# Optimization experiments

Measured on AMD Instinct MI355X. Metric: run time of the kernel, lower is better.

## Reference

```python
import jax, jax.numpy as jnp
import numpy as np

D_MODEL = 1024
HEADS = 16
HEAD_DIM = D_MODEL // HEADS
EPS = 1e-6


def feature_map(x):
    # F.elu(x) + 1
    return jax.nn.elu(x) + 1.0


def setup_inputs() -> dict:
    key = jax.random.key(0)
    ks = jax.random.split(key, 9)
    B, N, D = 4, 4096, D_MODEL
    s = 1.0 / np.sqrt(D)
    return {
        "x": jax.random.normal(ks[0], (B, N, D), dtype=jnp.float32),
        "Wq": jax.random.normal(ks[1], (D, D), dtype=jnp.float32) * s,
        "bq": jnp.zeros((D,), dtype=jnp.float32),
        "Wk": jax.random.normal(ks[2], (D, D), dtype=jnp.float32) * s,
        "bk": jnp.zeros((D,), dtype=jnp.float32),
        "Wv": jax.random.normal(ks[3], (D, D), dtype=jnp.float32) * s,
        "bv": jnp.zeros((D,), dtype=jnp.float32),
        "Wo": jax.random.normal(ks[4], (D, D), dtype=jnp.float32) * s,
        "bo": jnp.zeros((D,), dtype=jnp.float32),
    }


def reference(x, Wq, bq, Wk, bk, Wv, bv, Wo, bo):
    B, N, D = x.shape
    H, hd = HEADS, HEAD_DIM
    # torch Linear: y = x @ W.T + b
    q = feature_map((x @ Wq.T + bq).reshape(B, N, H, hd))
    k = feature_map((x @ Wk.T + bk).reshape(B, N, H, hd))
    v = (x @ Wv.T + bv).reshape(B, N, H, hd)
    k_sum = k.sum(axis=1)                                   # (B, H, hd)
    D_inv = 1.0 / (jnp.einsum('bnhd,bhd->bnh', q, k_sum) + EPS)
    context = jnp.einsum('bnhd,bnhv->bhdv', k, v)            # (B, H, hd, hd)
    out = jnp.einsum('bnhd,bhdv->bnhv', q, context) * D_inv[..., None]
    out = out.reshape(B, N, D)
    return out @ Wo.T + bo
```

## Files before the change

### kernel.cpp

```cpp
#include <hip/hip_runtime.h>
#include <hip/hip_bf16.h>

typedef __attribute__((ext_vector_type(8))) short bf16x8;
typedef __attribute__((ext_vector_type(4))) float f32x4;

__device__ __forceinline__ float b2f(unsigned short u) {
  union { unsigned int i; float f; } x; x.i = ((unsigned int)u) << 16; return x.f;
}
__device__ __forceinline__ unsigned short f2b(float f) {
  union { __hip_bfloat16 h; unsigned short u; } x; x.h = __float2bfloat16(f); return x.u;
}
__device__ __forceinline__ f32x4 mfma16(bf16x8 a, bf16x8 b, f32x4 c) {
  return __builtin_amdgcn_mfma_f32_16x16x32_bf16(a, b, c, 0, 0, 0);
}
__device__ __forceinline__ void gl16(const void* g, void* l) {
  __builtin_amdgcn_global_load_lds(
      (const __attribute__((address_space(1))) unsigned int*)g,
      (__attribute__((address_space(3))) unsigned int*)l, 16, 0, 0);
}

__global__ __launch_bounds__(256) void cast_k(const float* __restrict__ src,
                                              unsigned short* __restrict__ dst, int n4) {
  int i = blockIdx.x * 256 + threadIdx.x;
  if (i >= n4) return;
  float4 v = ((const float4*)src)[i];
  ushort4 o;
  o.x = f2b(v.x); o.y = f2b(v.y); o.z = f2b(v.z); o.w = f2b(v.w);
  ((ushort4*)dst)[i] = o;
}

__global__ __launch_bounds__(256) void castw_k(
    const float* __restrict__ s0, const float* __restrict__ s1,
    const float* __restrict__ s2, const float* __restrict__ s3,
    unsigned short* __restrict__ d0, unsigned short* __restrict__ d1,
    unsigned short* __restrict__ d2, unsigned short* __restrict__ d3) {
  int seg = blockIdx.x >> 10;
  int i = (blockIdx.x & 1023) * 256 + threadIdx.x;
  const float* s = (seg == 0) ? s0 : (seg == 1) ? s1 : (seg == 2) ? s2 : s3;
  unsigned short* d = (seg == 0) ? d0 : (seg == 1) ? d1 : (seg == 2) ? d2 : d3;
  float4 v = ((const float4*)s)[i];
  ushort4 o;
  o.x = f2b(v.x); o.y = f2b(v.y); o.z = f2b(v.z); o.w = f2b(v.w);
  ((ushort4*)d)[i] = o;
}

#define BARX() asm volatile("s_barrier" ::: "memory")
#define LGKM0() asm volatile("s_waitcnt lgkmcnt(0)" ::: "memory")
#define WAITV4() asm volatile("s_waitcnt vmcnt(4)" ::: "memory")
#define WAITV0() asm volatile("s_waitcnt vmcnt(0)" ::: "memory")
#define P1() __builtin_amdgcn_s_setprio(1)
#define P0() __builtin_amdgcn_s_setprio(0)

#define STAGE_A(BUF, G, TAU) do { \
  gl16(gA_0 + (size_t)(G) * 65536 + (TAU) * 64, sAB + (BUF) * 32768 + (G) * 16384 + u0 * 16); \
  gl16(gA_1 + (size_t)(G) * 65536 + (TAU) * 64, sAB + (BUF) * 32768 + (G) * 16384 + u1 * 16); } while (0)
#define STAGE_B(BUF, G, TAU) do { \
  gl16(gB_0 + (size_t)(G) * 32768 + (TAU) * 64, sAB + 65536 + (BUF) * 32768 + (G) * 16384 + u0 * 16); \
  gl16(gB_1 + (size_t)(G) * 32768 + (TAU) * 64, sAB + 65536 + (BUF) * 32768 + (G) * 16384 + u1 * 16); } while (0)

#define LOAD_A(BUF, MH) do { \
  _Pragma("unroll") for (int mi = 0; mi < 4; ++mi) { \
    const char* p_ = (const char*)sAB + (BUF) * 32768 + (MH) * 16384 + aRd + mi * 2048; \
    af[mi][0] = *(const bf16x8*)(p_ + sr0); \
    af[mi][1] = *(const bf16x8*)(p_ + sr1); } } while (0)
#define LOAD_B(BUF, NH, DST) do { \
  _Pragma("unroll") for (int ni = 0; ni < 2; ++ni) { \
    const char* p_ = (const char*)sAB + 65536 + (BUF) * 32768 + (NH) * 16384 + bRd + ni * 2048; \
    DST[ni][0] = *(const bf16x8*)(p_ + sr0); \
    DST[ni][1] = *(const bf16x8*)(p_ + sr1); } } while (0)

#define QUAD(MH, NH, BF) do { \
  _Pragma("unroll") for (int mi = 0; mi < 4; ++mi) \
    _Pragma("unroll") for (int ni = 0; ni < 2; ++ni) { \
      acc[(MH) * 4 + mi][(NH) * 2 + ni] = mfma16(af[mi][0], BF[ni][0], acc[(MH) * 4 + mi][(NH) * 2 + ni]); \
      acc[(MH) * 4 + mi][(NH) * 2 + ni] = mfma16(af[mi][1], BF[ni][1], acc[(MH) * 4 + mi][(NH) * 2 + ni]); } } while (0)

template<int MODE>
__global__ __launch_bounds__(512, 2) void gemm256(
    const unsigned short* __restrict__ A,
    const unsigned short* __restrict__ W0, const unsigned short* __restrict__ W1,
    const unsigned short* __restrict__ W2,
    const float* __restrict__ bias0, const float* __restrict__ bias1, const float* __restrict__ bias2,
    float* __restrict__ outF,
    unsigned short* __restrict__ o0, unsigned short* __restrict__ o1, unsigned short* __restrict__ o2,
    int tiles_n, float* __restrict__ ksum)
{
  __shared__ char sAB[131072];
  int bid = blockIdx.x;
  int nwg = gridDim.x;
  int cpx = nwg >> 3;
  int sbid = (bid & 7) * cpx + (bid >> 3);
  int tn = sbid % tiles_n, tm = sbid / tiles_n;
  int m0 = tm * 256, n0 = tn * 256;

  const unsigned short* W = W0; const float* bias = bias0; unsigned short* outB = o0;
  int sel = 0;
  if (MODE == 1) {
    sel = n0 >> 10;
    if (sel == 1) { W = W1; bias = bias1; outB = o1; }
    else if (sel == 2) { W = W2; bias = bias2; outB = o2; }
  } else {
    W = W0 + ((size_t)(m0 >> 12) << 20);
  }
  int nloc0 = (MODE == 1) ? (n0 & 1023) : n0;

  int t = threadIdx.x, w = t >> 6, l = t & 63;
  int wm = w >> 2, wn = w & 3;

  int u0 = t, u1 = t + 512;
  int lr0 = u0 >> 3, lr1 = u1 >> 3;
  int sl0 = (u0 & 7) ^ (lr0 & 7), sl1 = (u1 & 7) ^ (lr1 & 7);
  int rA0 = ((lr0 >> 6) << 7) + (lr0 & 63), rA1 = ((lr1 >> 6) << 7) + (lr1 & 63);
  int rB0 = ((lr0 >> 5) << 6) + (lr0 & 31), rB1 = ((lr1 >> 5) << 6) + (lr1 & 31);
  const unsigned short* gA_0 = A + (size_t)(m0 + rA0) * 1024 + sl0 * 8;
  const unsigned short* gA_1 = A + (size_t)(m0 + rA1) * 1024 + sl1 * 8;
  const unsigned short* gB_0 = W + (size_t)(nloc0 + rB0) * 1024 + sl0 * 8;
  const unsigned short* gB_1 = W + (size_t)(nloc0 + rB1) * 1024 + sl1 * 8;

  int aRd = (wm * 64 + (l & 15)) * 128;
  int bRd = (wn * 32 + (l & 15)) * 128;
  int sr0 = (((l >> 4) + 0) ^ (l & 7)) * 16;
  int sr1 = (((l >> 4) + 4) ^ (l & 7)) * 16;

  f32x4 acc[8][4];
  f32x4 zero = {0.f, 0.f, 0.f, 0.f};
#pragma unroll
  for (int i = 0; i < 8; ++i)
#pragma unroll
    for (int jx = 0; jx < 4; ++jx) acc[i][jx] = zero;
  bf16x8 af[4][2], bf0[2][2], bf1[2][2];

  STAGE_A(0, 0, 0); STAGE_B(0, 0, 0); STAGE_A(0, 1, 0); STAGE_B(0, 1, 0);
  STAGE_A(1, 0, 1); STAGE_B(1, 0, 1);
  WAITV4();
  BARX();

  for (int j = 0; j < 8; ++j) {
    int t1 = 2 * j + 1;
    int t2 = (j < 7) ? (2 * j + 2) : 14;
    int t3 = (j < 7) ? (2 * j + 3) : 15;
    LOAD_A(0, 0); LOAD_B(0, 0, bf0);
    STAGE_A(1, 1, t1);
    BARX(); LGKM0(); P1(); QUAD(0, 0, bf0); P0(); BARX();
    LOAD_B(0, 1, bf1);
    STAGE_B(1, 1, t1);
    BARX(); LGKM0(); P1(); QUAD(0, 1, bf1); P0(); BARX();
    LOAD_A(0, 1);
    STAGE_A(0, 0, t2);
    BARX(); LGKM0(); P1(); QUAD(1, 0, bf0); P0(); BARX();
    STAGE_B(0, 0, t2);
    BARX(); LGKM0(); P1(); QUAD(1, 1, bf1); P0(); WAITV4(); BARX();
    LOAD_A(1, 0); LOAD_B(1, 0, bf0);
    STAGE_A(0, 1, t2);
    BARX(); LGKM0(); P1(); QUAD(0, 0, bf0); P0(); BARX();
    LOAD_B(1, 1, bf1);
    STAGE_B(0, 1, t2);
    BARX(); LGKM0(); P1(); QUAD(0, 1, bf1); P0(); BARX();
    LOAD_A(1, 1);
    STAGE_A(1, 0, t3);
    BARX(); LGKM0(); P1(); QUAD(1, 0, bf0); P0(); BARX();
    STAGE_B(1, 0, t3);
    BARX(); LGKM0(); P1(); QUAD(1, 1, bf1); P0(); WAITV4(); BARX();
  }
  WAITV0();

  if (MODE == 1 && sel >= 1) {
    int b_idx = m0 >> 12;
    int nloc_h = nloc0 >> 6;
#pragma unroll
    for (int mq = 0; mq < 8; ++mq) {
      int r_base = wm * 128 + (mq >> 2) * 64 + (mq & 3) * 16 + ((l >> 4) << 2);
#pragma unroll
      for (int nq = 0; nq < 4; ++nq) {
        int c_loc = wn * 64 + (nq >> 1) * 32 + (nq & 1) * 16 + (l & 15);
        float bb = bias[nloc0 + c_loc];
        float v0 = acc[mq][nq][0] + bb, v1 = acc[mq][nq][1] + bb;
        float v2 = acc[mq][nq][2] + bb, v3 = acc[mq][nq][3] + bb;
        if (sel == 1) {
          v0 = (v0 > 0.0f) ? (v0 + 1.0f) : __expf(v0);
          v1 = (v1 > 0.0f) ? (v1 + 1.0f) : __expf(v1);
          v2 = (v2 > 0.0f) ? (v2 + 1.0f) : __expf(v2);
          v3 = (v3 > 0.0f) ? (v3 + 1.0f) : __expf(v3);
        }
        unsigned long long pk =
            (unsigned long long)(f2b(v0) | ((unsigned int)f2b(v1) << 16)) |
            ((unsigned long long)(f2b(v2) | ((unsigned int)f2b(v3) << 16)) << 32);
        int byte = c_loc * 512 + ((r_base * 2) ^ ((c_loc & 7) << 4));
        *(unsigned long long*)(sAB + byte) = pk;
      }
    }
    __syncthreads();
#pragma unroll
    for (int qq = 0; qq < 16; ++qq) {
      int c_loc = qq * 16 + w * 2 + (l >> 5);
      int n_off = (l & 31) * 8;
      int d = c_loc & 63;
      int bh = b_idx * 16 + nloc_h + (c_loc >> 6);
      int byte = c_loc * 512 + ((n_off * 2) ^ ((c_loc & 7) << 4));
      bf16x8 ch = *(const bf16x8*)(sAB + byte);
      *(bf16x8*)(outB + (size_t)(bh * 64 + d) * 4096 + (m0 & 4095) + n_off) = ch;
      if (sel == 1) {
        float s = 0.f;
#pragma unroll
        for (int jj = 0; jj < 8; ++jj) s += b2f((unsigned short)ch[jj]);
        s += __shfl_xor(s, 1);
        s += __shfl_xor(s, 2);
        s += __shfl_xor(s, 4);
        s += __shfl_xor(s, 8);
        s += __shfl_xor(s, 16);
        if ((l & 31) == 0) atomicAdd(ksum + bh * 64 + d, s);
      }
    }
  } else {
#pragma unroll
    for (int mq = 0; mq < 8; ++mq) {
      int grow = m0 + wm * 128 + (mq >> 2) * 64 + (mq & 3) * 16 + ((l >> 4) << 2);
#pragma unroll
      for (int nq = 0; nq < 4; ++nq) {
        int gcol = n0 + wn * 64 + (nq >> 1) * 32 + (nq & 1) * 16 + (l & 15);
        if (MODE == 0) {
          float bb = bias[gcol];
#pragma unroll
          for (int r = 0; r < 4; ++r)
            outF[(size_t)(grow + r) * 1024 + gcol] = acc[mq][nq][r] + bb;
        } else {
          int c = gcol & 1023;
          float bb = bias[c];
#pragma unroll
          for (int r = 0; r < 4; ++r) {
            float v = acc[mq][nq][r] + bb;
            v = (v > 0.0f) ? (v + 1.0f) : __expf(v);
            outB[(size_t)(grow + r) * 1024 + c] = f2b(v);
          }
        }
      }
    }
  }
}

__global__ __launch_bounds__(256) void ctx_gemm(
    const unsigned short* __restrict__ kT,
    const unsigned short* __restrict__ vT,
    float* __restrict__ ctxT)
{
  __shared__ float red[4][64 * 65];
  int bid = blockIdx.x;
  int bh = bid >> 3, ch = bid & 7;
  int t = threadIdx.x, wv = t >> 6, l = t & 63;
  int noff = ch * 512 + wv * 128 + ((l >> 4) << 3);
  const unsigned short* aB = kT + ((size_t)bh * 64 + (l & 15)) * 4096 + noff;
  const unsigned short* bB = vT + ((size_t)bh * 64 + (l & 15)) * 4096 + noff;
  f32x4 acc[4][4];
  f32x4 zero = {0.f, 0.f, 0.f, 0.f};
#pragma unroll
  for (int i = 0; i < 4; ++i)
#pragma unroll
    for (int j = 0; j < 4; ++j) acc[i][j] = zero;
  for (int ks = 0; ks < 4; ++ks) {
    bf16x8 av[4], bv[4];
#pragma unroll
    for (int mi = 0; mi < 4; ++mi) av[mi] = *(const bf16x8*)(aB + (size_t)mi * 16 * 4096 + ks * 32);
#pragma unroll
    for (int ni = 0; ni < 4; ++ni) bv[ni] = *(const bf16x8*)(bB + (size_t)ni * 16 * 4096 + ks * 32);
#pragma unroll
    for (int mi = 0; mi < 4; ++mi)
#pragma unroll
      for (int ni = 0; ni < 4; ++ni)
        acc[mi][ni] = mfma16(av[mi], bv[ni], acc[mi][ni]);
  }
#pragma unroll
  for (int mi = 0; mi < 4; ++mi)
#pragma unroll
    for (int ni = 0; ni < 4; ++ni)
#pragma unroll
      for (int r = 0; r < 4; ++r) {
        int dd = mi * 16 + ((l >> 4) << 2) + r;
        int vv = ni * 16 + (l & 15);
        red[wv][dd * 65 + vv] = acc[mi][ni][r];
      }
  __syncthreads();
  for (int o = t; o < 4096; o += 256) {
    int idx = (o >> 6) * 65 + (o & 63);
    float s = red[0][idx] + red[1][idx] + red[2][idx] + red[3][idx];
    atomicAdd(ctxT + (size_t)bh * 4096 + o, s);
  }
}

__global__ __launch_bounds__(1024) void ctxwo_k(
    const float* __restrict__ ctxT,
    const unsigned short* __restrict__ wo,
    unsigned short* __restrict__ M)
{
  int bh = blockIdx.x;
  int b = bh >> 4, h = bh & 15;
  int t = threadIdx.x, wv = t >> 6, l = t & 63;
  int j0 = wv * 64;

  bf16x8 af[4][2], bf[4][2];
#pragma unroll
  for (int mi = 0; mi < 4; ++mi)
#pragma unroll
    for (int ks = 0; ks < 2; ++ks)
      af[mi][ks] = *(const bf16x8*)(wo + (size_t)(j0 + mi * 16 + (l & 15)) * 1024 +
                                    h * 64 + ((l >> 4) << 3) + ks * 32);
#pragma unroll
  for (int ni = 0; ni < 4; ++ni)
#pragma unroll
    for (int ks = 0; ks < 2; ++ks) {
      const float* p = ctxT + (size_t)bh * 4096 + (ni * 16 + (l & 15)) * 64 +
                       ((l >> 4) << 3) + ks * 32;
#pragma unroll
      for (int jj = 0; jj < 8; ++jj) bf[ni][ks][jj] = (short)f2b(p[jj]);
    }

  f32x4 acc[4][4];
  f32x4 zero = {0.f, 0.f, 0.f, 0.f};
#pragma unroll
  for (int i = 0; i < 4; ++i)
#pragma unroll
    for (int j = 0; j < 4; ++j) acc[i][j] = zero;
#pragma unroll
  for (int mi = 0; mi < 4; ++mi)
#pragma unroll
    for (int ni = 0; ni < 4; ++ni) {
      acc[mi][ni] = mfma16(af[mi][0], bf[ni][0], acc[mi][ni]);
      acc[mi][ni] = mfma16(af[mi][1], bf[ni][1], acc[mi][ni]);
    }

  unsigned short* Mb = M + ((size_t)b << 20);
#pragma unroll
  for (int mi = 0; mi < 4; ++mi)
#pragma unroll
    for (int ni = 0; ni < 4; ++ni)
#pragma unroll
      for (int r = 0; r < 4; ++r) {
        int j = j0 + mi * 16 + ((l >> 4) << 2) + r;
        int d = ni * 16 + (l & 15);
        Mb[(size_t)j * 1024 + h * 64 + d] = f2b(acc[mi][ni][r]);
      }
}

__global__ __launch_bounds__(256) void dinvq_k(
    unsigned short* __restrict__ q,
    const float* __restrict__ ksum)
{
  int t = threadIdx.x, wv = t >> 6, l = t & 63;
  int n = blockIdx.x * 4 + wv;
  int b = n >> 12;
  int h = l >> 2;
  unsigned short* qp = q + (size_t)n * 1024 + l * 16;
  const float* kp = ksum + (b * 16 + h) * 64 + (l & 3) * 16;
  bf16x8 v0 = *(const bf16x8*)qp;
  bf16x8 v1 = *(const bf16x8*)(qp + 8);
  float s = 0.f;
#pragma unroll
  for (int j = 0; j < 8; ++j) {
    s += b2f((unsigned short)v0[j]) * kp[j];
    s += b2f((unsigned short)v1[j]) * kp[8 + j];
  }
  s += __shfl_xor(s, 1);
  s += __shfl_xor(s, 2);
  float di = 1.0f / (s + 1e-6f);
#pragma unroll
  for (int j = 0; j < 8; ++j) {
    v0[j] = (short)f2b(b2f((unsigned short)v0[j]) * di);
    v1[j] = (short)f2b(b2f((unsigned short)v1[j]) * di);
  }
  *(bf16x8*)qp = v0;
  *(bf16x8*)(qp + 8) = v1;
}

extern "C" void kernel_launch(void* const* d_in, const int* in_sizes, int n_in,
                              void* d_out, int out_size, void* d_ws, size_t ws_size,
                              hipStream_t stream)
{
  const float* x  = (const float*)d_in[0];
  const float* bq = (const float*)d_in[2];
  const float* bk = (const float*)d_in[4];
  const float* bv = (const float*)d_in[6];
  const float* bo = (const float*)d_in[8];
  const float* Wq = (const float*)d_in[1];
  const float* Wk = (const float*)d_in[3];
  const float* Wv = (const float*)d_in[5];
  const float* Wo = (const float*)d_in[7];
  float* out = (float*)d_out;

  char* ws = (char*)d_ws;
  const size_t SB = (size_t)16384 * 1024 * 2;
  const size_t NEED = 4 * SB + 4 * (1u << 21) + 2 * (1u << 20) + (1u << 14);
  if (ws_size < NEED) return;

  unsigned short* xb  = (unsigned short*)(ws);
  unsigned short* qb  = (unsigned short*)(ws + SB);
  unsigned short* kTb = (unsigned short*)(ws + 2 * SB);
  unsigned short* vTb = (unsigned short*)(ws + 3 * SB);
  unsigned short* wqb = (unsigned short*)(ws + 4 * SB);
  unsigned short* wkb = (unsigned short*)(ws + 4 * SB + (1u << 21));
  unsigned short* wvb = (unsigned short*)(ws + 4 * SB + (2u << 21));
  unsigned short* wob = (unsigned short*)(ws + 4 * SB + (3u << 21));
  float* ctxT = (float*)(ws + 4 * SB + (4u << 21));
  float* ksum = (float*)(ws + 4 * SB + (4u << 21) + (2u << 20));
  unsigned short* Mbuf = xb;

  hipMemsetAsync(ctxT, 0, 64 * 64 * 64 * 4, stream);
  hipMemsetAsync(ksum, 0, 64 * 64 * 4, stream);

  cast_k<<<16384, 256, 0, stream>>>(x, xb, 16777216 / 4);
  castw_k<<<4096, 256, 0, stream>>>(Wq, Wk, Wv, Wo, wqb, wkb, wvb, wob);

  gemm256<1><<<768, 512, 0, stream>>>(xb, wqb, wkb, wvb, bq, bk, bv,
                                      nullptr, qb, kTb, vTb, 12, ksum);

  ctx_gemm<<<512, 256, 0, stream>>>(kTb, vTb, ctxT);

  ctxwo_k<<<64, 1024, 0, stream>>>(ctxT, wob, Mbuf);

  dinvq_k<<<4096, 256, 0, stream>>>(qb, ksum);

  gemm256<0><<<256, 512, 0, stream>>>(qb, Mbuf, nullptr, nullptr, bo, nullptr, nullptr,
                                      out, nullptr, nullptr, nullptr, 4, nullptr);
}
```

Baseline: 229.8 us.

## Drop memsets and atomics for context; move barriers after fragment loads

Removes both hipMemsetAsync launches. The ksum buffer is now zeroed by an extra block of the weight-cast kernel. ctx_gemm writes per-chunk partial context tiles to a scratch region instead of using atomicAdd, and ctxwo_k sums the eight partials into shared memory before use. In the main GEMM loop, the barrier after some MFMA quads is moved past the next LDS fragment load, so the loads overlap with the quad instead of waiting on a barrier. The scratch region sits inside the xb buffer at an 8 MB offset, which is assumed to be dead after the QKV GEMM.

```diff
diff --git a/kernel.cpp b/kernel.cpp
--- a/kernel.cpp
+++ b/kernel.cpp
@@ -33,7 +33,15 @@
     const float* __restrict__ s0, const float* __restrict__ s1,
     const float* __restrict__ s2, const float* __restrict__ s3,
     unsigned short* __restrict__ d0, unsigned short* __restrict__ d1,
-    unsigned short* __restrict__ d2, unsigned short* __restrict__ d3) {
+    unsigned short* __restrict__ d2, unsigned short* __restrict__ d3,
+    float* __restrict__ ksum) {
+  if (blockIdx.x == 4096) {
+    ((float4*)ksum)[threadIdx.x * 4 + 0] = make_float4(0.f, 0.f, 0.f, 0.f);
+    ((float4*)ksum)[threadIdx.x * 4 + 1] = make_float4(0.f, 0.f, 0.f, 0.f);
+    ((float4*)ksum)[threadIdx.x * 4 + 2] = make_float4(0.f, 0.f, 0.f, 0.f);
+    ((float4*)ksum)[threadIdx.x * 4 + 3] = make_float4(0.f, 0.f, 0.f, 0.f);
+    return;
+  }
   int seg = blockIdx.x >> 10;
   int i = (blockIdx.x & 1023) * 256 + threadIdx.x;
   const float* s = (seg == 0) ? s0 : (seg == 1) ? s1 : (seg == 2) ? s2 : s3;
@@ -141,22 +149,26 @@
     int t3 = (j < 7) ? (2 * j + 3) : 15;
     LOAD_A(0, 0); LOAD_B(0, 0, bf0);
     STAGE_A(1, 1, t1);
-    BARX(); LGKM0(); P1(); QUAD(0, 0, bf0); P0(); BARX();
+    BARX(); LGKM0(); P1(); QUAD(0, 0, bf0); P0();
     LOAD_B(0, 1, bf1);
+    BARX();
     STAGE_B(1, 1, t1);
-    BARX(); LGKM0(); P1(); QUAD(0, 1, bf1); P0(); BARX();
+    BARX(); LGKM0(); P1(); QUAD(0, 1, bf1); P0();
     LOAD_A(0, 1);
+    BARX();
     STAGE_A(0, 0, t2);
     BARX(); LGKM0(); P1(); QUAD(1, 0, bf0); P0(); BARX();
     STAGE_B(0, 0, t2);
     BARX(); LGKM0(); P1(); QUAD(1, 1, bf1); P0(); WAITV4(); BARX();
     LOAD_A(1, 0); LOAD_B(1, 0, bf0);
     STAGE_A(0, 1, t2);
-    BARX(); LGKM0(); P1(); QUAD(0, 0, bf0); P0(); BARX();
+    BARX(); LGKM0(); P1(); QUAD(0, 0, bf0); P0();
     LOAD_B(1, 1, bf1);
+    BARX();
     STAGE_B(0, 1, t2);
-    BARX(); LGKM0(); P1(); QUAD(0, 1, bf1); P0(); BARX();
+    BARX(); LGKM0(); P1(); QUAD(0, 1, bf1); P0();
     LOAD_A(1, 1);
+    BARX();
     STAGE_A(1, 0, t3);
     BARX(); LGKM0(); P1(); QUAD(1, 0, bf0); P0(); BARX();
     STAGE_B(1, 0, t3);
@@ -241,7 +253,7 @@
 __global__ __launch_bounds__(256) void ctx_gemm(
     const unsigned short* __restrict__ kT,
     const unsigned short* __restrict__ vT,
-    float* __restrict__ ctxT)
+    float* __restrict__ ctxP)
 {
   __shared__ float red[4][64 * 65];
   int bid = blockIdx.x;
@@ -281,21 +293,29 @@
   __syncthreads();
   for (int o = t; o < 4096; o += 256) {
     int idx = (o >> 6) * 65 + (o & 63);
-    float s = red[0][idx] + red[1][idx] + red[2][idx] + red[3][idx];
-    atomicAdd(ctxT + (size_t)bh * 4096 + o, s);
+    ctxP[(size_t)bid * 4096 + o] = red[0][idx] + red[1][idx] + red[2][idx] + red[3][idx];
   }
 }
 
 __global__ __launch_bounds__(1024) void ctxwo_k(
-    const float* __restrict__ ctxT,
+    const float* __restrict__ ctxP,
     const unsigned short* __restrict__ wo,
     unsigned short* __restrict__ M)
 {
+  __shared__ float cs[4096];
   int bh = blockIdx.x;
   int b = bh >> 4, h = bh & 15;
   int t = threadIdx.x, wv = t >> 6, l = t & 63;
   int j0 = wv * 64;
 
+  for (int o = t; o < 4096; o += 1024) {
+    float s = 0.f;
+#pragma unroll
+    for (int ch = 0; ch < 8; ++ch) s += ctxP[((size_t)bh * 8 + ch) * 4096 + o];
+    cs[o] = s;
+  }
+  __syncthreads();
+
   bf16x8 af[4][2], bf[4][2];
 #pragma unroll
   for (int mi = 0; mi < 4; ++mi)
@@ -307,8 +327,7 @@
   for (int ni = 0; ni < 4; ++ni)
 #pragma unroll
     for (int ks = 0; ks < 2; ++ks) {
-      const float* p = ctxT + (size_t)bh * 4096 + (ni * 16 + (l & 15)) * 64 +
-                       ((l >> 4) << 3) + ks * 32;
+      const float* p = cs + (ni * 16 + (l & 15)) * 64 + ((l >> 4) << 3) + ks * 32;
 #pragma unroll
       for (int jj = 0; jj < 8; ++jj) bf[ni][ks][jj] = (short)f2b(p[jj]);
     }
@@ -398,22 +417,19 @@
   unsigned short* wkb = (unsigned short*)(ws + 4 * SB + (1u << 21));
   unsigned short* wvb = (unsigned short*)(ws + 4 * SB + (2u << 21));
   unsigned short* wob = (unsigned short*)(ws + 4 * SB + (3u << 21));
-  float* ctxT = (float*)(ws + 4 * SB + (4u << 21));
   float* ksum = (float*)(ws + 4 * SB + (4u << 21) + (2u << 20));
   unsigned short* Mbuf = xb;
-
-  hipMemsetAsync(ctxT, 0, 64 * 64 * 64 * 4, stream);
-  hipMemsetAsync(ksum, 0, 64 * 64 * 4, stream);
+  float* ctxP = (float*)(ws + (8u << 20));
 
   cast_k<<<16384, 256, 0, stream>>>(x, xb, 16777216 / 4);
-  castw_k<<<4096, 256, 0, stream>>>(Wq, Wk, Wv, Wo, wqb, wkb, wvb, wob);
+  castw_k<<<4097, 256, 0, stream>>>(Wq, Wk, Wv, Wo, wqb, wkb, wvb, wob, ksum);
 
   gemm256<1><<<768, 512, 0, stream>>>(xb, wqb, wkb, wvb, bq, bk, bv,
                                       nullptr, qb, kTb, vTb, 12, ksum);
 
-  ctx_gemm<<<512, 256, 0, stream>>>(kTb, vTb, ctxT);
-
-  ctxwo_k<<<64, 1024, 0, stream>>>(ctxT, wob, Mbuf);
+  ctx_gemm<<<512, 256, 0, stream>>>(kTb, vTb, ctxP);
+
+  ctxwo_k<<<64, 1024, 0, stream>>>(ctxP, wob, Mbuf);
 
   dinvq_k<<<4096, 256, 0, stream>>>(qb, ksum);
 
```

Measured after the change: 220.0 us. -4.3%, faster.
